# Optimization experiments

Measured on AMD Instinct MI355X. Metric: run time of the kernel, lower is better.

The kernel has to match this reference:

```python
import jax, jax.numpy as jnp
import numpy as np

H, B, N, D, VD, FFH = 8, 16, 512, 512, 64, 2048
NPICK = N // 2
NORM = 1.0 / np.sqrt(VD)


def _ha_encoder(h, W_query, W_key, W_val, W1, W2, W3, W4, W5, W6):
    # h: [B, N, D]; weights: [H, D, VD]
    np_ = NPICK
    pick, dlv = h[:, :np_], h[:, np_:]
    proj = lambda x, W: jnp.einsum('bnd,hdk->hbnk', x, W)
    Q, K, V = proj(h, W_query), proj(h, W_key), proj(h, W_val)
    Kp, Kd = K[:, :, :np_], K[:, :, np_:]   # shared projections (same W_key)
    Vp, Vd = V[:, :, :np_], V[:, :, np_:]
    Qp = proj(pick, W1); Qpap = proj(pick, W2); Qpad = proj(pick, W3)
    Qd = proj(dlv, W4);  Qdad = proj(dlv, W5);  Qdap = proj(dlv, W6)
    c_main = NORM * jnp.einsum('hbnk,hbmk->hbnm', Q, K)          # [H,B,N,N]
    c_pd = NORM * jnp.sum(Qp * Kd, -1)                           # [H,B,np] paired pick->delivery
    c_pap = NORM * jnp.einsum('hbnk,hbmk->hbnm', Qpap, Kp)       # pick -> all pick
    c_pad = NORM * jnp.einsum('hbnk,hbmk->hbnm', Qpad, Kd)       # pick -> all delivery
    c_dp = NORM * jnp.sum(Qd * Kp, -1)                           # paired delivery->pick
    c_dad = NORM * jnp.einsum('hbnk,hbmk->hbnm', Qdad, Kd)       # delivery -> all delivery
    c_dap = NORM * jnp.einsum('hbnk,hbmk->hbnm', Qdap, Kp)       # delivery -> all pick
    ninf1 = jnp.full((H, h.shape[0], np_), -jnp.inf, c_main.dtype)
    ninf2 = jnp.full((H, h.shape[0], np_, np_), -jnp.inf, c_main.dtype)
    col_pd = jnp.concatenate([c_pd, ninf1], 2)[..., None]        # [H,B,N,1]
    blk_pap = jnp.concatenate([c_pap, ninf2], 2)                 # [H,B,N,np]
    blk_pad = jnp.concatenate([c_pad, ninf2], 2)
    col_dp = jnp.concatenate([ninf1, c_dp], 2)[..., None]
    blk_dad = jnp.concatenate([ninf2, c_dad], 2)
    blk_dap = jnp.concatenate([ninf2, c_dap], 2)
    compat = jnp.concatenate([c_main, col_pd, blk_pap, blk_pad, col_dp, blk_dad, blk_dap], -1)
    a = jax.nn.softmax(compat, -1)                               # [H,B,N,N+2+4*np]
    zpad = jnp.zeros_like(Vd)
    V_add_d = jnp.concatenate([Vd, zpad], 2)                     # [H,B,N,VD]
    V_add_p = jnp.concatenate([zpad, Vp], 2)
    av = lambda w, v: jnp.einsum('hbnm,hbmv->hbnv', w, v)
    i = N
    heads = av(a[..., :N], V)
    heads = heads + a[..., i:i + 1] * V_add_d; i += 1
    heads = heads + av(a[..., i:i + np_], Vp); i += np_
    heads = heads + av(a[..., i:i + np_], Vd); i += np_
    heads = heads + a[..., i:i + 1] * V_add_p; i += 1
    heads = heads + av(a[..., i:i + np_], Vd); i += np_
    heads = heads + av(a[..., i:i + np_], Vp)
    return heads.transpose(1, 2, 0, 3).reshape(h.shape[0], N, H * VD)


def _split_heads(x):
    b, n, hd = x.shape
    return x.reshape(b, n, H, hd // H).transpose(0, 2, 1, 3)


def _mha(q, k, v):
    dk = q.shape[-1]
    w = jax.nn.softmax(jnp.einsum('bhnd,bhmd->bhnm', q, k) / np.sqrt(dk), -1)
    o = jnp.einsum('bhnm,bhmd->bhnd', w, v)
    b, hh, n, d = o.shape
    return o.transpose(0, 2, 1, 3).reshape(b, n, hh * d)


def _ff(x, w1, b1, w2, b2, a):
    return x + (jax.nn.relu(x @ w1 + b1) @ w2 + b2) * a


def _forward(x, W_query, W_key, W_val, W1_query, W2_query, W3_query, W4_query, W5_query, W6_query,
             Wq_w, Wk_w, Wv_w, Wq2p_w, Wq2d_w, Wk2_w, Wv2_w,
             comb_w, comb_b, comb2_w, comb2_b, comb3_w, comb3_b,
             alpha1, alpha2, alpha3,
             ff1_w1, ff1_b1, ff1_w2, ff1_b2, ffa1,
             ff2_w1, ff2_b1, ff2_w2, ff2_b2, ffa2,
             ff3_w1, ff3_b1, ff3_w2, ff3_b2, ffa3):
    # stage 1: heterogeneous attention block (combine_3 / AN3 / FF3)
    ha = _ha_encoder(x, W_query, W_key, W_val, W1_query, W2_query, W3_query, W4_query, W5_query, W6_query)
    out = x + (ha @ comb3_w + comb3_b) * alpha3
    out = _ff(out, ff3_w1, ff3_b1, ff3_w2, ff3_b2, ffa3)
    # stage 2: standard multi-head self-attention (combine / AN1 / FF1)
    q = _split_heads(out @ Wq_w); k = _split_heads(out @ Wk_w); v = _split_heads(out @ Wv_w)
    out = out + (_mha(q, k, v) @ comb_w + comb_b) * alpha1
    out = _ff(out, ff1_w1, ff1_b1, ff1_w2, ff1_b2, ffa1)
    # stage 3: pickup/delivery specific queries (combine_2 / AN2 / FF2)
    q2 = jnp.concatenate([out[:, :NPICK] @ Wq2p_w, out[:, NPICK:] @ Wq2d_w], 1)
    q2 = _split_heads(q2); k2 = _split_heads(out @ Wk2_w); v2 = _split_heads(out @ Wv2_w)
    out = out + (_mha(q2, k2, v2) @ comb2_w + comb2_b) * alpha2
    out = _ff(out, ff2_w1, ff2_b1, ff2_w2, ff2_b2, ffa2)
    return out


def setup_inputs() -> dict:
    key = jax.random.key(0)
    ks = jax.random.split(key, 64)
    it = iter(range(64))
    def nrm(shape):
        return jax.random.normal(ks[next(it)], shape, jnp.float32)
    def uni(shape):
        s = 1.0 / np.sqrt(shape[-1])  # torch init_parameters: uniform(-1/sqrt(size(-1)), ...)
        return jax.random.uniform(ks[next(it)], shape, jnp.float32, -s, s)
    d = {'x': nrm((B, N, D))}
    for n in ['W_query', 'W_key', 'W_val', 'W1_query', 'W2_query', 'W3_query', 'W4_query', 'W5_query', 'W6_query']:
        d[n] = uni((H, D, VD))
    for n in ['Wq_w', 'Wk_w', 'Wv_w', 'Wq2p_w', 'Wq2d_w', 'Wk2_w', 'Wv2_w']:
        d[n] = uni((D, H * VD))
    for n in ['comb_w', 'comb2_w', 'comb3_w']:
        d[n] = uni((H * VD, D))
    for n in ['comb_b', 'comb2_b', 'comb3_b']:
        d[n] = uni((D,))
    for n in ['alpha1', 'alpha2', 'alpha3']:
        d[n] = uni((1,))
    for i in ['1', '2', '3']:
        d['ff' + i + '_w1'] = uni((D, FFH))
        d['ff' + i + '_b1'] = uni((FFH,))
        d['ff' + i + '_w2'] = uni((FFH, D))
        d['ff' + i + '_b2'] = uni((D,))
        d['ffa' + i] = uni((1,))
    return d


def reference(x, W_query, W_key, W_val, W1_query, W2_query, W3_query, W4_query, W5_query, W6_query,
              Wq_w, Wk_w, Wv_w, Wq2p_w, Wq2d_w, Wk2_w, Wv2_w,
              comb_w, comb_b, comb2_w, comb2_b, comb3_w, comb3_b,
              alpha1, alpha2, alpha3,
              ff1_w1, ff1_b1, ff1_w2, ff1_b2, ffa1,
              ff2_w1, ff2_b1, ff2_w2, ff2_b2, ffa2,
              ff3_w1, ff3_b1, ff3_w2, ff3_b2, ffa3):
    return _forward(x, W_query, W_key, W_val, W1_query, W2_query, W3_query, W4_query, W5_query, W6_query,
                    Wq_w, Wk_w, Wv_w, Wq2p_w, Wq2d_w, Wk2_w, Wv2_w,
                    comb_w, comb_b, comb2_w, comb2_b, comb3_w, comb3_b,
                    alpha1, alpha2, alpha3,
                    ff1_w1, ff1_b1, ff1_w2, ff1_b2, ffa1,
                    ff2_w1, ff2_b1, ff2_w2, ff2_b2, ffa2,
                    ff3_w1, ff3_b1, ff3_w2, ff3_b2, ffa3)
```

## Files before the change

### kernel.cpp

```cpp
#include <hip/hip_runtime.h>
#include <math.h>

#define Hh 8
#define Bb 16
#define Nn 512
#define Dd 512
#define VDd 64
#define NPICKk 256
#define NORMF 0.125f
#define SCL2 0.1803368801f

typedef unsigned short ushortT;
typedef __bf16 bf16x8 __attribute__((ext_vector_type(8)));
typedef float f32x4 __attribute__((ext_vector_type(4)));

struct PtrsB { const ushortT* p[12]; };
struct PtrsD { ushortT* p[6]; };
struct Ptrs9 { const float* p[9]; };
struct Ptrs10 { const float* p[10]; };
struct Ptrs6 { const float* p[6]; };

__device__ inline ushortT f2bf(float f) {
    __bf16 h = (__bf16)f;
    union { __bf16 h; ushortT u; } v; v.h = h;
    return v.u;
}
__device__ inline float bf2f(ushortT u) {
    union { unsigned int u; float f; } v; v.u = ((unsigned int)u) << 16;
    return v.f;
}
__device__ inline float exp2fast(float x) {
#if __has_builtin(__builtin_amdgcn_exp2f)
    return __builtin_amdgcn_exp2f(x);
#else
    return exp2f(x);
#endif
}
__device__ inline void gload16(const void* gptr, void* ldsptr) {
    auto g = reinterpret_cast<const __attribute__((address_space(1))) unsigned int*>(
        reinterpret_cast<uintptr_t>(gptr));
    auto l = reinterpret_cast<__attribute__((address_space(3))) unsigned int*>(
        reinterpret_cast<uintptr_t>(ldsptr));
    __builtin_amdgcn_global_load_lds(g, l, 16, 0, 0);
}

#define LIX(r, g) (((r) << 6) + ((((g) ^ ((r) & 7))) << 3))

__global__ __launch_bounds__(256) void castx(const float* __restrict__ in,
                                             ushortT* __restrict__ out) {
    int i = blockIdx.x * 256 + threadIdx.x;
    float4 v = *(const float4*)&in[(size_t)i * 4];
    ushort4 o; o.x = f2bf(v.x); o.y = f2bf(v.y); o.z = f2bf(v.z); o.w = f2bf(v.w);
    *(ushort4*)&out[(size_t)i * 4] = o;
}

__device__ inline void tbody(const float* __restrict__ in, ushortT* __restrict__ out,
                             int in_ld, int out_ld, int r0, int c0) {
    __shared__ float T[64][65];
    int tr = threadIdx.x >> 4, tc4 = (threadIdx.x & 15) * 4;
#pragma unroll
    for (int p = 0; p < 4; ++p) {
        float4 v = *(const float4*)&in[(size_t)(r0 + tr + p * 16) * in_ld + c0 + tc4];
        T[tr + p * 16][tc4 + 0] = v.x; T[tr + p * 16][tc4 + 1] = v.y;
        T[tr + p * 16][tc4 + 2] = v.z; T[tr + p * 16][tc4 + 3] = v.w;
    }
    __syncthreads();
#pragma unroll
    for (int p = 0; p < 4; ++p) {
        int orow = c0 + tr + p * 16;
        int ocol = r0 + tc4;
        ushort4 o;
        o.x = f2bf(T[tc4 + 0][tr + p * 16]);
        o.y = f2bf(T[tc4 + 1][tr + p * 16]);
        o.z = f2bf(T[tc4 + 2][tr + p * 16]);
        o.w = f2bf(T[tc4 + 3][tr + p * 16]);
        *(ushort4*)&out[(size_t)orow * out_ld + ocol] = o;
    }
}

__global__ __launch_bounds__(256) void thead(Ptrs9 s, ushortT* __restrict__ dst) {
    int w = blockIdx.z >> 3, h = blockIdx.z & 7;
    tbody(s.p[w] + (size_t)h * 512 * 64,
          dst + (size_t)w * 262144 + (size_t)h * 64 * 512,
          64, 512, blockIdx.y * 64, 0);
}
__global__ __launch_bounds__(256) void tsq(Ptrs10 s, ushortT* __restrict__ dst) {
    tbody(s.p[blockIdx.z], dst + (size_t)blockIdx.z * 262144,
          512, 512, blockIdx.y * 64, blockIdx.x * 64);
}
__global__ __launch_bounds__(256) void tff(Ptrs6 s, ushortT* __restrict__ dst) {
    int z = blockIdx.z;
    if (z < 3) { if (blockIdx.y >= 8 || blockIdx.x >= 32) return; }
    else       { if (blockIdx.y >= 32 || blockIdx.x >= 8) return; }
    int in_ld = (z < 3) ? 2048 : 512;
    int out_ld = (z < 3) ? 512 : 2048;
    tbody(s.p[z], dst + (size_t)z * 1048576, in_ld, out_ld,
          blockIdx.y * 64, blockIdx.x * 64);
}

__global__ __launch_bounds__(256) void gemm_bf(
    PtrsB Bp, PtrsD Db, const ushortT* __restrict__ A, float* __restrict__ outF,
    int M, int N, int K, const float* __restrict__ bias,
    const float* __restrict__ res, const float* __restrict__ alpha,
    int do_relu, int nroute, int vtmask, int scmask)
{
    __shared__ __align__(16) ushortT As[2][128 * 64];
    __shared__ __align__(16) ushortT Bs[2][128 * 64];
    const int tid = threadIdx.x;
    const int wid = tid >> 6, lane = tid & 63;
    const int wm = wid >> 1, wn = wid & 1;
    const int l15 = lane & 15, l4 = lane >> 4;

    int bid = blockIdx.y * gridDim.x + blockIdx.x;
    int nwg = gridDim.x * gridDim.y;
    int q = nwg >> 3;
    int swz = (bid & 7) * q + (bid >> 3);
    int bx = swz % gridDim.x, by = swz / gridDim.x;

    const int r0 = by * 128, c0 = bx * 128;
    const int half = ((r0 & (Nn - 1)) >= NPICKk) ? 1 : 0;
    const ushortT* Bt = Bp.p[((c0 >> 9) << 1) | half];
    const int cB = nroute ? (c0 & 511) : c0;

    const ushortT* aSrc[4];
    const ushortT* bSrc[4];
    int offv[4];
#pragma unroll
    for (int i = 0; i < 4; ++i) {
        int off = wid * 4096 + i * 1024 + lane * 16;
        int row = off >> 7;
        int sg = ((off >> 4) & 7) ^ (row & 7);
        aSrc[i] = A + (size_t)(r0 + row) * K + sg * 8;
        bSrc[i] = Bt + (size_t)(cB + row) * K + sg * 8;
        offv[i] = off;
    }

    const int nkt = K >> 6;
#pragma unroll
    for (int i = 0; i < 4; ++i) {
        gload16(aSrc[i], (char*)As[0] + offv[i]);
        gload16(bSrc[i], (char*)Bs[0] + offv[i]);
    }
#pragma unroll
    for (int i = 0; i < 4; ++i) {
        gload16(aSrc[i] + 64, (char*)As[1] + offv[i]);
        gload16(bSrc[i] + 64, (char*)Bs[1] + offv[i]);
    }

    f32x4 acc[4][4] = {};

    for (int t = 0; t < nkt; ++t) {
        const int cur = t & 1;
        if (t == nkt - 1) asm volatile("s_waitcnt vmcnt(0)" ::: "memory");
        else              asm volatile("s_waitcnt vmcnt(8)" ::: "memory");
        __builtin_amdgcn_s_barrier();
        __builtin_amdgcn_sched_barrier(0);
        const ushortT* Ac = As[cur];
        const ushortT* Bc = Bs[cur];
        __builtin_amdgcn_s_setprio(1);
#pragma unroll
        for (int kk = 0; kk < 2; ++kk) {
            int g0 = kk * 4 + l4;
            bf16x8 af[4], bfv[4];
#pragma unroll
            for (int mi = 0; mi < 4; ++mi)
                af[mi] = *(const bf16x8*)&Ac[LIX(wm * 64 + mi * 16 + l15, g0)];
#pragma unroll
            for (int ni = 0; ni < 4; ++ni)
                bfv[ni] = *(const bf16x8*)&Bc[LIX(wn * 64 + ni * 16 + l15, g0)];
#pragma unroll
            for (int mi = 0; mi < 4; ++mi)
#pragma unroll
                for (int ni = 0; ni < 4; ++ni)
                    acc[mi][ni] = __builtin_amdgcn_mfma_f32_16x16x32_bf16(
                        bfv[ni], af[mi], acc[mi][ni], 0, 0, 0);
        }
        __builtin_amdgcn_s_setprio(0);
        __builtin_amdgcn_s_barrier();
        asm volatile("" ::: "memory");
        if (t + 2 < nkt) {
            int kt2 = (t + 2) << 6;
#pragma unroll
            for (int i = 0; i < 4; ++i) {
                gload16(aSrc[i] + kt2, (char*)As[cur] + offv[i]);
                gload16(bSrc[i] + kt2, (char*)Bs[cur] + offv[i]);
            }
        }
    }

    if (nroute) {
#pragma unroll
        for (int mi = 0; mi < 4; ++mi) {
            int row = r0 + wm * 64 + mi * 16 + l15;
#pragma unroll
            for (int ni = 0; ni < 4; ++ni) {
                int col = c0 + wn * 64 + ni * 16 + l4 * 4;
                int range = col >> 9, cc = col & 511;
                ushortT* d = Db.p[range];
                f32x4 a = acc[mi][ni];
                if ((scmask >> range) & 1) {
                    a[0] *= SCL2; a[1] *= SCL2; a[2] *= SCL2; a[3] *= SCL2;
                }
                if ((vtmask >> range) & 1) {
                    size_t vb = ((size_t)(row >> 9) * Hh + (cc >> 6)) * 64 + (cc & 63);
                    int tok = row & 511;
#pragma unroll
                    for (int r = 0; r < 4; ++r)
                        d[((vb + r) << 9) + tok] = f2bf(a[r]);
                } else {
                    ushort4 o;
                    o.x = f2bf(a[0]); o.y = f2bf(a[1]);
                    o.z = f2bf(a[2]); o.w = f2bf(a[3]);
                    *(ushort4*)&d[((size_t)row << 9) + cc] = o;
                }
            }
        }
    } else {
        const float alp = alpha ? alpha[0] : 1.0f;
        ushortT* outB = Db.p[0];
#pragma unroll
        for (int mi = 0; mi < 4; ++mi) {
            int row = r0 + wm * 64 + mi * 16 + l15;
#pragma unroll
            for (int ni = 0; ni < 4; ++ni) {
                int colb = c0 + wn * 64 + ni * 16 + l4 * 4;
                f32x4 a = acc[mi][ni];
                if (bias) {
                    float4 b4 = *(const float4*)&bias[colb];
                    a[0] += b4.x; a[1] += b4.y; a[2] += b4.z; a[3] += b4.w;
                }
                if (do_relu) {
#pragma unroll
                    for (int r = 0; r < 4; ++r) a[r] = fmaxf(a[r], 0.f);
                }
#pragma unroll
                for (int r = 0; r < 4; ++r) a[r] *= alp;
                size_t idx = (size_t)row * N + colb;
                if (res) {
                    float4 r4 = *(const float4*)&res[idx];
                    a[0] += r4.x; a[1] += r4.y; a[2] += r4.z; a[3] += r4.w;
                }
                if (outF)
                    *(float4*)&outF[idx] = make_float4(a[0], a[1], a[2], a[3]);
                if (outB) {
                    ushort4 o;
                    o.x = f2bf(a[0]); o.y = f2bf(a[1]);
                    o.z = f2bf(a[2]); o.w = f2bf(a[3]);
                    *(ushort4*)&outB[idx] = o;
                }
            }
        }
    }
}

__global__ __launch_bounds__(256) void gemm64(
    const ushortT* __restrict__ Bw, const ushortT* __restrict__ A,
    float* __restrict__ outF, ushortT* __restrict__ outB,
    int M, int N, int K, const float* __restrict__ bias,
    const float* __restrict__ resf, const ushortT* __restrict__ resb,
    const float* __restrict__ alpha, int do_relu)
{
    __shared__ __align__(16) ushortT As[2][64 * 64];
    __shared__ __align__(16) ushortT Bs[2][128 * 64];
    const int tid = threadIdx.x;
    const int wid = tid >> 6, lane = tid & 63;
    const int wm = wid >> 1, wn = wid & 1;
    const int l15 = lane & 15, l4 = lane >> 4;

    int bid = blockIdx.y * gridDim.x + blockIdx.x;
    int nwg = gridDim.x * gridDim.y;
    int q = nwg >> 3;
    int swz = (bid & 7) * q + (bid >> 3);
    int bx = swz % gridDim.x, by = swz / gridDim.x;
    const int r0 = by * 64, c0 = bx * 128;

    const ushortT* aSrc[2];
    int offA[2];
#pragma unroll
    for (int i = 0; i < 2; ++i) {
        int off = wid * 2048 + i * 1024 + lane * 16;
        int row = off >> 7;
        int sg = ((off >> 4) & 7) ^ (row & 7);
        aSrc[i] = A + (size_t)(r0 + row) * K + sg * 8;
        offA[i] = off;
    }
    const ushortT* bSrc[4];
    int offB[4];
#pragma unroll
    for (int i = 0; i < 4; ++i) {
        int off = wid * 4096 + i * 1024 + lane * 16;
        int row = off >> 7;
        int sg = ((off >> 4) & 7) ^ (row & 7);
        bSrc[i] = Bw + (size_t)(c0 + row) * K + sg * 8;
        offB[i] = off;
    }

    const int nkt = K >> 6;
#pragma unroll
    for (int i = 0; i < 2; ++i) gload16(aSrc[i], (char*)As[0] + offA[i]);
#pragma unroll
    for (int i = 0; i < 4; ++i) gload16(bSrc[i], (char*)Bs[0] + offB[i]);
#pragma unroll
    for (int i = 0; i < 2; ++i) gload16(aSrc[i] + 64, (char*)As[1] + offA[i]);
#pragma unroll
    for (int i = 0; i < 4; ++i) gload16(bSrc[i] + 64, (char*)Bs[1] + offB[i]);

    f32x4 acc[2][4] = {};

    for (int t = 0; t < nkt; ++t) {
        const int cur = t & 1;
        if (t == nkt - 1) asm volatile("s_waitcnt vmcnt(0)" ::: "memory");
        else              asm volatile("s_waitcnt vmcnt(6)" ::: "memory");
        __builtin_amdgcn_s_barrier();
        __builtin_amdgcn_sched_barrier(0);
        const ushortT* Ac = As[cur];
        const ushortT* Bc = Bs[cur];
        __builtin_amdgcn_s_setprio(1);
#pragma unroll
        for (int kk = 0; kk < 2; ++kk) {
            int g0 = kk * 4 + l4;
            bf16x8 af[2], bfv[4];
#pragma unroll
            for (int mi = 0; mi < 2; ++mi)
                af[mi] = *(const bf16x8*)&Ac[LIX(wm * 32 + mi * 16 + l15, g0)];
#pragma unroll
            for (int ni = 0; ni < 4; ++ni)
                bfv[ni] = *(const bf16x8*)&Bc[LIX(wn * 64 + ni * 16 + l15, g0)];
#pragma unroll
            for (int mi = 0; mi < 2; ++mi)
#pragma unroll
                for (int ni = 0; ni < 4; ++ni)
                    acc[mi][ni] = __builtin_amdgcn_mfma_f32_16x16x32_bf16(
                        bfv[ni], af[mi], acc[mi][ni], 0, 0, 0);
        }
        __builtin_amdgcn_s_setprio(0);
        __builtin_amdgcn_s_barrier();
        asm volatile("" ::: "memory");
        if (t + 2 < nkt) {
            int kt2 = (t + 2) << 6;
#pragma unroll
            for (int i = 0; i < 2; ++i) gload16(aSrc[i] + kt2, (char*)As[cur] + offA[i]);
#pragma unroll
            for (int i = 0; i < 4; ++i) gload16(bSrc[i] + kt2, (char*)Bs[cur] + offB[i]);
        }
    }

    const float alp = alpha ? alpha[0] : 1.0f;
#pragma unroll
    for (int mi = 0; mi < 2; ++mi) {
        int row = r0 + wm * 32 + mi * 16 + l15;
#pragma unroll
        for (int ni = 0; ni < 4; ++ni) {
            int colb = c0 + wn * 64 + ni * 16 + l4 * 4;
            f32x4 a = acc[mi][ni];
            if (bias) {
                float4 b4 = *(const float4*)&bias[colb];
                a[0] += b4.x; a[1] += b4.y; a[2] += b4.z; a[3] += b4.w;
            }
            if (do_relu) {
#pragma unroll
                for (int r = 0; r < 4; ++r) a[r] = fmaxf(a[r], 0.f);
            }
#pragma unroll
            for (int r = 0; r < 4; ++r) a[r] *= alp;
            size_t idx = (size_t)row * N + colb;
            if (resf) {
                float4 r4 = *(const float4*)&resf[idx];
                a[0] += r4.x; a[1] += r4.y; a[2] += r4.z; a[3] += r4.w;
            }
            if (resb) {
                ushort4 r4 = *(const ushort4*)&resb[idx];
                a[0] += bf2f(r4.x); a[1] += bf2f(r4.y);
                a[2] += bf2f(r4.z); a[3] += bf2f(r4.w);
            }
            if (outF)
                *(float4*)&outF[idx] = make_float4(a[0], a[1], a[2], a[3]);
            if (outB) {
                ushort4 o;
                o.x = f2bf(a[0]); o.y = f2bf(a[1]);
                o.z = f2bf(a[2]); o.w = f2bf(a[3]);
                *(ushort4*)&outB[idx] = o;
            }
        }
    }
}

__global__ __launch_bounds__(256) void diag_dot_bb(const ushortT* __restrict__ QD,
                                                   const ushortT* __restrict__ K,
                                                   float* __restrict__ Sdg) {
    int i = blockIdx.x * 256 + threadIdx.x;
    int h = i & 7, n = (i >> 3) & 511, b = i >> 12;
    int dix = (n < NPICKk) ? n + NPICKk : n - NPICKk;
    const ushortT* q = QD + (((size_t)(b * Nn + n) * Hh + h) << 6);
    const ushortT* k = K + (((size_t)(b * Nn + dix) * Hh + h) << 6);
    float s = 0.f;
#pragma unroll
    for (int d = 0; d < 64; d += 4) {
        ushort4 a = *(const ushort4*)(q + d);
        ushort4 c = *(const ushort4*)(k + d);
        s += bf2f(a.x) * bf2f(c.x) + bf2f(a.y) * bf2f(c.y)
           + bf2f(a.z) * bf2f(c.z) + bf2f(a.w) * bf2f(c.w);
    }
    Sdg[i] = s;
}

template <int HA>
__global__ __launch_bounds__(256) void attn10(
    const ushortT* __restrict__ Qm, const ushortT* __restrict__ Km,
    const ushortT* __restrict__ Vtm, const ushortT* __restrict__ QAm,
    const ushortT* __restrict__ QBm, const float* __restrict__ Sdg,
    ushortT* __restrict__ Out)
{
    __shared__ __align__(16) ushortT Ks[64 * 64];
    __shared__ __align__(16) ushortT Vs[64 * 64];
    __shared__ __align__(16) ushortT Pw[4][16 * 64];
    __shared__ float sdl[64];

    const int tid = threadIdx.x, wid = tid >> 6, lane = tid & 63;
    const int l15 = lane & 15, l4 = lane >> 4;

    const int p = blockIdx.x + (blockIdx.y << 3) + (blockIdx.z << 6);
    const int n0 = (((p >> 3) & 7)) << 6;
    const int g8 = (p & 7) | ((p >> 6) << 3);
    const int h = g8 & 7, b = g8 >> 3;
    const int bh = b * Hh + h;

    const size_t qrow = (((size_t)(b * Nn + n0 + wid * 16 + l15) * Hh + h) << 6);
    bf16x8 qf[2], xaf[2], xbf[2];
#pragma unroll
    for (int kk = 0; kk < 2; ++kk) {
        int g0 = kk * 4 + l4;
        qf[kk] = *(const bf16x8*)&Qm[qrow + g0 * 8];
        if (HA) {
            xaf[kk] = *(const bf16x8*)&QAm[qrow + g0 * 8];
            xbf[kk] = *(const bf16x8*)&QBm[qrow + g0 * 8];
        }
    }
    if (HA && tid < 64) sdl[tid] = Sdg[((size_t)(b * Nn + n0 + tid)) * Hh + h];
    const int td = (n0 < NPICKk) ? ((n0 + NPICKk) >> 6) : ((n0 - NPICKk) >> 6);

    const ushortT* kSrc[2]; ushortT* kDst[2];
    const ushortT* vSrc[2]; ushortT* vDst[2];
#pragma unroll
    for (int i = 0; i < 2; ++i) {
        int off = wid * 2048 + i * 1024 + lane * 16;
        int row = off >> 7, sg = ((off >> 4) & 7) ^ (row & 7);
        kSrc[i] = Km + (((size_t)(b * Nn + row) * Hh + h) << 6) + sg * 8;
        kDst[i] = (ushortT*)((char*)Ks + off);
        vSrc[i] = Vtm + (((size_t)(bh * 64 + row)) << 9) + sg * 8;
        vDst[i] = (ushortT*)((char*)Vs + off);
    }

    float M[4], Lp[4];
    f32x4 Oa[4] = {};
#pragma unroll
    for (int r = 0; r < 4; ++r) { M[r] = -INFINITY; Lp[r] = 0.f; }

    bf16x8 krbuf[2][2], vrbuf[2][2];
#pragma unroll
    for (int i = 0; i < 2; ++i) {
        krbuf[0][i] = *(const bf16x8*)kSrc[i];
        vrbuf[0][i] = *(const bf16x8*)vSrc[i];
    }

#pragma unroll
    for (int t = 0; t < 8; ++t) {
        const int cur = t & 1, nxt = cur ^ 1;
        __builtin_amdgcn_s_barrier();
#pragma unroll
        for (int i = 0; i < 2; ++i) {
            *(bf16x8*)kDst[i] = krbuf[cur][i];
            *(bf16x8*)vDst[i] = vrbuf[cur][i];
        }
        if (t < 7) {
#pragma unroll
            for (int i = 0; i < 2; ++i) {
                krbuf[nxt][i] = *(const bf16x8*)(kSrc[i] + (size_t)(t + 1) * (64 * Hh * VDd));
                vrbuf[nxt][i] = *(const bf16x8*)(vSrc[i] + (t + 1) * 64);
            }
        }
        asm volatile("s_waitcnt lgkmcnt(0)" ::: "memory");
        __builtin_amdgcn_s_barrier();
        __builtin_amdgcn_sched_barrier(0);

        __builtin_amdgcn_s_setprio(1);
        f32x4 s1[4] = {}, sX[4] = {};
#pragma unroll
        for (int kk = 0; kk < 2; ++kk) {
            bf16x8 aq = qf[kk];
            bf16x8 ax;
            if (HA) ax = (t >= 4) ? xbf[kk] : xaf[kk];
#pragma unroll
            for (int ni = 0; ni < 4; ++ni) {
                bf16x8 bk = *(const bf16x8*)&Ks[LIX(ni * 16 + l15, kk * 4 + l4)];
                s1[ni] = __builtin_amdgcn_mfma_f32_16x16x32_bf16(aq, bk, s1[ni], 0, 0, 0);
                if (HA)
                    sX[ni] = __builtin_amdgcn_mfma_f32_16x16x32_bf16(ax, bk, sX[ni], 0, 0, 0);
            }
        }
        __builtin_amdgcn_s_setprio(0);

        const bool dt = HA && (t == td);

        float mloc[4];
        bool grow = false;
#pragma unroll
        for (int r = 0; r < 4; ++r) {
            int rw = wid * 16 + l4 * 4 + r;
            float m = s1[0][r];
#pragma unroll
            for (int ni = 1; ni < 4; ++ni) m = fmaxf(m, s1[ni][r]);
            if (HA) {
#pragma unroll
                for (int ni = 0; ni < 4; ++ni) m = fmaxf(m, sX[ni][r]);
            }
            if (dt && l15 == l4 * 4 + r) m = fmaxf(m, sdl[rw]);
            mloc[r] = m;
            grow = grow || (m > M[r] + 8.f);
        }
        if (__any(grow)) {
#pragma unroll
            for (int r = 0; r < 4; ++r) {
                float m = mloc[r];
#pragma unroll
                for (int o = 8; o >= 1; o >>= 1) m = fmaxf(m, __shfl_xor(m, o, 16));
                float mn = fmaxf(M[r], m);
                float sc = exp2fast(M[r] - mn);
                M[r] = mn; Lp[r] *= sc;
#pragma unroll
                for (int ni = 0; ni < 4; ++ni) Oa[ni][r] *= sc;
            }
        }

#pragma unroll
        for (int r = 0; r < 4; ++r) {
            int rw = wid * 16 + l4 * 4 + r;
            float rs = 0.f;
#pragma unroll
            for (int ni = 0; ni < 4; ++ni) {
                float pv = exp2fast(s1[ni][r] - M[r]);
                if (HA) pv += exp2fast(sX[ni][r] - M[r]);
                if (dt && ni == wid && l15 == l4 * 4 + r) pv += exp2fast(sdl[rw] - M[r]);
                s1[ni][r] = pv;
                rs += pv;
            }
            Lp[r] += rs;
        }

#pragma unroll
        for (int ni = 0; ni < 4; ++ni)
#pragma unroll
            for (int r = 0; r < 4; ++r) {
                int prow = l4 * 4 + r;
                int col = ni * 16 + l15;
                Pw[wid][(prow << 6) + ((((col >> 3) ^ (prow & 7))) << 3) + (col & 7)] =
                    f2bf(s1[ni][r]);
            }

        __builtin_amdgcn_s_setprio(1);
#pragma unroll
        for (int kk = 0; kk < 2; ++kk) {
            int g0 = kk * 4 + l4;
            bf16x8 ap = *(const bf16x8*)&Pw[wid][LIX(l15, g0)];
#pragma unroll
            for (int ni = 0; ni < 4; ++ni) {
                bf16x8 bv = *(const bf16x8*)&Vs[LIX(ni * 16 + l15, g0)];
                Oa[ni] = __builtin_amdgcn_mfma_f32_16x16x32_bf16(ap, bv, Oa[ni], 0, 0, 0);
            }
        }
        __builtin_amdgcn_s_setprio(0);
    }

#pragma unroll
    for (int r = 0; r < 4; ++r) {
        float l = Lp[r];
#pragma unroll
        for (int o = 8; o >= 1; o >>= 1) l += __shfl_xor(l, o, 16);
        float inv = 1.0f / l;
        size_t obase = (((size_t)(b * Nn + n0 + wid * 16 + l4 * 4 + r) * Hh + h) << 6);
#pragma unroll
        for (int ni = 0; ni < 4; ++ni)
            Out[obase + ni * 16 + l15] = f2bf(Oa[ni][r] * inv);
    }
}

extern "C" void kernel_launch(void* const* d_in, const int* in_sizes, int n_in,
                              void* d_out, int out_size, void* d_ws, size_t ws_size,
                              hipStream_t stream)
{
    const float* x = (const float*)d_in[0];

    int dictOrder = (in_sizes[18] != 512);
    const float* comb_w  = (const float*)d_in[17];
    const float* comb2_w = (const float*)d_in[dictOrder ? 18 : 19];
    const float* comb3_w = (const float*)d_in[dictOrder ? 19 : 21];
    const float* comb_b  = (const float*)d_in[dictOrder ? 20 : 18];
    const float* comb2_b = (const float*)d_in[dictOrder ? 21 : 20];
    const float* comb3_b = (const float*)d_in[22];
    const float* alpha1 = (const float*)d_in[23];
    const float* alpha2 = (const float*)d_in[24];
    const float* alpha3 = (const float*)d_in[25];
    const float* ff1_w1 = (const float*)d_in[26];
    const float* ff1_b1 = (const float*)d_in[27];
    const float* ff1_w2 = (const float*)d_in[28];
    const float* ff1_b2 = (const float*)d_in[29];
    const float* ffa1   = (const float*)d_in[30];
    const float* ff2_w1 = (const float*)d_in[31];
    const float* ff2_b1 = (const float*)d_in[32];
    const float* ff2_w2 = (const float*)d_in[33];
    const float* ff2_b2 = (const float*)d_in[34];
    const float* ffa2   = (const float*)d_in[35];
    const float* ff3_w1 = (const float*)d_in[36];
    const float* ff3_b1 = (const float*)d_in[37];
    const float* ff3_w2 = (const float*)d_in[38];
    const float* ff3_b2 = (const float*)d_in[39];
    const float* ffa3   = (const float*)d_in[40];

    char* W = (char*)d_ws;
    ushortT* wbHead = (ushortT*)(W + 0);
    ushortT* wbMha  = (ushortT*)(W + 4718592);
    ushortT* wbComb = (ushortT*)(W + 8388608);
    ushortT* wbFf1  = (ushortT*)(W + 9961472);
    ushortT* wbFf2  = (ushortT*)(W + 16252928);
    ushortT* xbf    = (ushortT*)(W + 22544384);
    float*   Sd     = (float*)  (W + 30932992);
    ushortT* bufQ   = (ushortT*)(W + 31195136);
    ushortT* bufK   = (ushortT*)(W + 39583744);
    ushortT* bufVt  = (ushortT*)(W + 47972352);
    ushortT* bufQA  = (ushortT*)(W + 56360960);
    ushortT* bufQB  = (ushortT*)(W + 64749568);
    ushortT* bufQD  = (ushortT*)(W + 73138176);
    ushortT* hidden = (ushortT*)(W + 81526784);
    ushortT* curb   = (ushortT*)(W + 115081216);
    ushortT* bufHA  = xbf;
    float*   cur    = (float*)d_out;

    dim3 tb(256);
    const int TOK = Bb * Nn;
    const size_t WS = 512 * 512;
    const size_t WF = 2048 * 512;

    hipLaunchKernelGGL(castx, dim3(TOK * 512 / 1024), tb, 0, stream, x, xbf);
    {
        Ptrs9 s; for (int i = 0; i < 9; ++i) s.p[i] = (const float*)d_in[1 + i];
        hipLaunchKernelGGL(thead, dim3(1, 8, 72), tb, 0, stream, s, wbHead);
    }
    {
        Ptrs10 s;
        for (int i = 0; i < 7; ++i) s.p[i] = (const float*)d_in[10 + i];
        s.p[7] = comb_w; s.p[8] = comb2_w; s.p[9] = comb3_w;
        hipLaunchKernelGGL(tsq, dim3(8, 8, 10), tb, 0, stream, s, wbMha);
    }
    {
        Ptrs6 s;
        s.p[0] = ff1_w1; s.p[1] = ff2_w1; s.p[2] = ff3_w1;
        s.p[3] = ff1_w2; s.p[4] = ff2_w2; s.p[5] = ff3_w2;
        hipLaunchKernelGGL(tff, dim3(32, 32, 6), tb, 0, stream, s, wbFf1);
    }

    auto gemm = [&](PtrsB Bp, PtrsD Db, const ushortT* A, float* oF,
                    int M, int Ncc, int Kc, const float* bias, const float* res,
                    const float* alp, int relu, int nroute, int vtmask, int scmask) {
        hipLaunchKernelGGL(gemm_bf, dim3(Ncc / 128, M / 128), tb, 0, stream,
                           Bp, Db, A, oF, M, Ncc, Kc, bias, res, alp, relu, nroute,
                           vtmask, scmask);
    };
    auto g64 = [&](const ushortT* Bw, const ushortT* A, float* oF, ushortT* oB,
                   int M, int Ncc, int Kc, const float* bias, const float* resf,
                   const ushortT* resb, const float* alp, int relu) {
        hipLaunchKernelGGL(gemm64, dim3(Ncc / 128, M / 64), tb, 0, stream,
                           Bw, A, oF, oB, M, Ncc, Kc, bias, resf, resb, alp, relu);
    };
    auto uni = [&](const ushortT* w) { PtrsB b; for (int i = 0; i < 12; ++i) b.p[i] = w; return b; };
    auto d1 = [&](ushortT* d) { PtrsD dd = {}; dd.p[0] = d; return dd; };

    {
        PtrsB b;
        b.p[0] = b.p[1] = wbHead + 0 * WS;
        b.p[2] = b.p[3] = wbHead + 1 * WS;
        b.p[4] = b.p[5] = wbHead + 2 * WS;
        b.p[6] = wbHead + 4 * WS; b.p[7] = wbHead + 8 * WS;
        b.p[8] = wbHead + 5 * WS; b.p[9] = wbHead + 7 * WS;
        b.p[10] = wbHead + 3 * WS; b.p[11] = wbHead + 6 * WS;
        PtrsD d; d.p[0] = bufQ; d.p[1] = bufK; d.p[2] = bufVt;
        d.p[3] = bufQA; d.p[4] = bufQB; d.p[5] = bufQD;
        gemm(b, d, xbf, nullptr, TOK, 3072, 512, nullptr, nullptr, nullptr, 0, 6, 4, 57);
    }

    hipLaunchKernelGGL(diag_dot_bb, dim3(Bb * Nn * Hh / 256), tb, 0, stream, bufQD, bufK, Sd);
    hipLaunchKernelGGL((attn10<1>), dim3(Nn / 64, Hh, Bb), tb, 0, stream,
                       bufQ, bufK, bufVt, bufQA, bufQB, Sd, bufHA);

    g64(wbComb + 2 * WS, bufHA, nullptr, curb, TOK, 512, 512, comb3_b, x, nullptr, alpha3, 0);
    gemm(uni(wbFf1 + 2 * WF), d1(hidden), curb, nullptr, TOK, 2048, 512, ff3_b1, nullptr, nullptr, 1, 0, 0, 0);
    g64(wbFf2 + 2 * WF, hidden, nullptr, curb, TOK, 512, 2048, ff3_b2, nullptr, curb, ffa3, 0);

    {
        PtrsB b;
        b.p[0] = b.p[1] = wbMha + 0 * WS;
        b.p[2] = b.p[3] = wbMha + 1 * WS;
        b.p[4] = b.p[5] = wbMha + 2 * WS;
        PtrsD d = {}; d.p[0] = bufQ; d.p[1] = bufK; d.p[2] = bufVt;
        gemm(b, d, curb, nullptr, TOK, 1536, 512, nullptr, nullptr, nullptr, 0, 3, 4, 1);
    }
    hipLaunchKernelGGL((attn10<0>), dim3(Nn / 64, Hh, Bb), tb, 0, stream,
                       bufQ, bufK, bufVt, nullptr, nullptr, nullptr, bufHA);
    g64(wbComb + 0 * WS, bufHA, nullptr, curb, TOK, 512, 512, comb_b, nullptr, curb, alpha1, 0);
    gemm(uni(wbFf1 + 0 * WF), d1(hidden), curb, nullptr, TOK, 2048, 512, ff1_b1, nullptr, nullptr, 1, 0, 0, 0);
    g64(wbFf2 + 0 * WF, hidden, nullptr, curb, TOK, 512, 2048, ff1_b2, nullptr, curb, ffa1, 0);

    {
        PtrsB b;
        b.p[0] = wbMha + 3 * WS; b.p[1] = wbMha + 4 * WS;
        b.p[2] = b.p[3] = wbMha + 5 * WS;
        b.p[4] = b.p[5] = wbMha + 6 * WS;
        PtrsD d = {}; d.p[0] = bufQ; d.p[1] = bufK; d.p[2] = bufVt;
        gemm(b, d, curb, nullptr, TOK, 1536, 512, nullptr, nullptr, nullptr, 0, 3, 4, 1);
    }
    hipLaunchKernelGGL((attn10<0>), dim3(Nn / 64, Hh, Bb), tb, 0, stream,
                       bufQ, bufK, bufVt, nullptr, nullptr, nullptr, bufHA);
    g64(wbComb + 1 * WS, bufHA, nullptr, curb, TOK, 512, 512, comb2_b, nullptr, curb, alpha2, 0);
    gemm(uni(wbFf1 + 1 * WF), d1(hidden), curb, nullptr, TOK, 2048, 512, ff2_b1, nullptr, nullptr, 1, 0, 0, 0);
    g64(wbFf2 + 1 * WF, hidden, cur, nullptr, TOK, 512, 2048, ff2_b2, nullptr, curb, ffa2, 0);
}
```

Before: 426.4 us.

## Double attention query tile to 128 rows with 512-thread blocks sharing K/V

Each attention block now covers 128 query rows with 8 waves instead of 64 rows with 4, so every K/V tile staged in shared memory serves twice as many queries and each thread issues half as many global loads per tile. The grid shrinks to 512 blocks, and the diagonal-term indexing is adjusted per wave group. The cost is fewer blocks to spread across CUs and more waves waiting at each barrier.

```diff
diff --git a/kernel.cpp b/kernel.cpp
--- a/kernel.cpp
+++ b/kernel.cpp
@@ -405,7 +405,7 @@
 }
 
 template <int HA>
-__global__ __launch_bounds__(256) void attn10(
+__global__ __launch_bounds__(512) void attn11(
     const ushortT* __restrict__ Qm, const ushortT* __restrict__ Km,
     const ushortT* __restrict__ Vtm, const ushortT* __restrict__ QAm,
     const ushortT* __restrict__ QBm, const float* __restrict__ Sdg,
@@ -413,15 +413,15 @@
 {
     __shared__ __align__(16) ushortT Ks[64 * 64];
     __shared__ __align__(16) ushortT Vs[64 * 64];
-    __shared__ __align__(16) ushortT Pw[4][16 * 64];
-    __shared__ float sdl[64];
+    __shared__ __align__(16) ushortT Pw[8][16 * 64];
+    __shared__ float sdl[128];
 
     const int tid = threadIdx.x, wid = tid >> 6, lane = tid & 63;
     const int l15 = lane & 15, l4 = lane >> 4;
 
-    const int p = blockIdx.x + (blockIdx.y << 3) + (blockIdx.z << 6);
-    const int n0 = (((p >> 3) & 7)) << 6;
-    const int g8 = (p & 7) | ((p >> 6) << 3);
+    const int p = blockIdx.x + (blockIdx.y << 2) + (blockIdx.z << 5);
+    const int n0 = ((p >> 3) & 3) << 7;
+    const int g8 = (p & 7) | ((p >> 5) << 3);
     const int h = g8 & 7, b = g8 >> 3;
     const int bh = b * Hh + h;
 
@@ -436,48 +436,35 @@
             xbf[kk] = *(const bf16x8*)&QBm[qrow + g0 * 8];
         }
     }
-    if (HA && tid < 64) sdl[tid] = Sdg[((size_t)(b * Nn + n0 + tid)) * Hh + h];
-    const int td = (n0 < NPICKk) ? ((n0 + NPICKk) >> 6) : ((n0 - NPICKk) >> 6);
-
-    const ushortT* kSrc[2]; ushortT* kDst[2];
-    const ushortT* vSrc[2]; ushortT* vDst[2];
-#pragma unroll
-    for (int i = 0; i < 2; ++i) {
-        int off = wid * 2048 + i * 1024 + lane * 16;
-        int row = off >> 7, sg = ((off >> 4) & 7) ^ (row & 7);
-        kSrc[i] = Km + (((size_t)(b * Nn + row) * Hh + h) << 6) + sg * 8;
-        kDst[i] = (ushortT*)((char*)Ks + off);
-        vSrc[i] = Vtm + (((size_t)(bh * 64 + row)) << 9) + sg * 8;
-        vDst[i] = (ushortT*)((char*)Vs + off);
-    }
+    if (HA && tid < 128) sdl[tid] = Sdg[((size_t)(b * Nn + n0 + tid)) * Hh + h];
+    const int n0g = n0 + ((wid >> 2) << 6);
+    const int td = (n0g < NPICKk) ? ((n0g + NPICKk) >> 6) : ((n0g - NPICKk) >> 6);
+
+    const int off = wid * 1024 + lane * 16;
+    const int srow = off >> 7, sg = ((off >> 4) & 7) ^ (srow & 7);
+    const ushortT* kSrc = Km + (((size_t)(b * Nn + srow) * Hh + h) << 6) + sg * 8;
+    ushortT* kDst = (ushortT*)((char*)Ks + off);
+    const ushortT* vSrc = Vtm + (((size_t)(bh * 64 + srow)) << 9) + sg * 8;
+    ushortT* vDst = (ushortT*)((char*)Vs + off);
 
     float M[4], Lp[4];
     f32x4 Oa[4] = {};
 #pragma unroll
     for (int r = 0; r < 4; ++r) { M[r] = -INFINITY; Lp[r] = 0.f; }
 
-    bf16x8 krbuf[2][2], vrbuf[2][2];
-#pragma unroll
-    for (int i = 0; i < 2; ++i) {
-        krbuf[0][i] = *(const bf16x8*)kSrc[i];
-        vrbuf[0][i] = *(const bf16x8*)vSrc[i];
-    }
+    bf16x8 krbuf[2], vrbuf[2];
+    krbuf[0] = *(const bf16x8*)kSrc;
+    vrbuf[0] = *(const bf16x8*)vSrc;
 
 #pragma unroll
     for (int t = 0; t < 8; ++t) {
         const int cur = t & 1, nxt = cur ^ 1;
         __builtin_amdgcn_s_barrier();
-#pragma unroll
-        for (int i = 0; i < 2; ++i) {
-            *(bf16x8*)kDst[i] = krbuf[cur][i];
-            *(bf16x8*)vDst[i] = vrbuf[cur][i];
-        }
+        *(bf16x8*)kDst = krbuf[cur];
+        *(bf16x8*)vDst = vrbuf[cur];
         if (t < 7) {
-#pragma unroll
-            for (int i = 0; i < 2; ++i) {
-                krbuf[nxt][i] = *(const bf16x8*)(kSrc[i] + (size_t)(t + 1) * (64 * Hh * VDd));
-                vrbuf[nxt][i] = *(const bf16x8*)(vSrc[i] + (t + 1) * 64);
-            }
+            krbuf[nxt] = *(const bf16x8*)(kSrc + (size_t)(t + 1) * (64 * Hh * VDd));
+            vrbuf[nxt] = *(const bf16x8*)(vSrc + (t + 1) * 64);
         }
         asm volatile("s_waitcnt lgkmcnt(0)" ::: "memory");
         __builtin_amdgcn_s_barrier();
@@ -540,7 +527,8 @@
             for (int ni = 0; ni < 4; ++ni) {
                 float pv = exp2fast(s1[ni][r] - M[r]);
                 if (HA) pv += exp2fast(sX[ni][r] - M[r]);
-                if (dt && ni == wid && l15 == l4 * 4 + r) pv += exp2fast(sdl[rw] - M[r]);
+                if (dt && ni == (wid & 3) && l15 == l4 * 4 + r)
+                    pv += exp2fast(sdl[rw] - M[r]);
                 s1[ni][r] = pv;
                 rs += pv;
             }
@@ -688,7 +676,7 @@
     }
 
     hipLaunchKernelGGL(diag_dot_bb, dim3(Bb * Nn * Hh / 256), tb, 0, stream, bufQD, bufK, Sd);
-    hipLaunchKernelGGL((attn10<1>), dim3(Nn / 64, Hh, Bb), tb, 0, stream,
+    hipLaunchKernelGGL((attn11<1>), dim3(Nn / 128, Hh, Bb), dim3(512), 0, stream,
                        bufQ, bufK, bufVt, bufQA, bufQB, Sd, bufHA);
 
     g64(wbComb + 2 * WS, bufHA, nullptr, curb, TOK, 512, 512, comb3_b, x, nullptr, alpha3, 0);
@@ -703,7 +691,7 @@
         PtrsD d = {}; d.p[0] = bufQ; d.p[1] = bufK; d.p[2] = bufVt;
         gemm(b, d, curb, nullptr, TOK, 1536, 512, nullptr, nullptr, nullptr, 0, 3, 4, 1);
     }
-    hipLaunchKernelGGL((attn10<0>), dim3(Nn / 64, Hh, Bb), tb, 0, stream,
+    hipLaunchKernelGGL((attn11<0>), dim3(Nn / 128, Hh, Bb), dim3(512), 0, stream,
                        bufQ, bufK, bufVt, nullptr, nullptr, nullptr, bufHA);
     g64(wbComb + 0 * WS, bufHA, nullptr, curb, TOK, 512, 512, comb_b, nullptr, curb, alpha1, 0);
     gemm(uni(wbFf1 + 0 * WF), d1(hidden), curb, nullptr, TOK, 2048, 512, ff1_b1, nullptr, nullptr, 1, 0, 0, 0);
@@ -717,7 +705,7 @@
         PtrsD d = {}; d.p[0] = bufQ; d.p[1] = bufK; d.p[2] = bufVt;
         gemm(b, d, curb, nullptr, TOK, 1536, 512, nullptr, nullptr, nullptr, 0, 3, 4, 1);
     }
-    hipLaunchKernelGGL((attn10<0>), dim3(Nn / 64, Hh, Bb), tb, 0, stream,
+    hipLaunchKernelGGL((attn11<0>), dim3(Nn / 128, Hh, Bb), dim3(512), 0, stream,
                        bufQ, bufK, bufVt, nullptr, nullptr, nullptr, bufHA);
     g64(wbComb + 1 * WS, bufHA, nullptr, curb, TOK, 512, 512, comb2_b, nullptr, curb, alpha2, 0);
     gemm(uni(wbFf1 + 1 * WF), d1(hidden), curb, nullptr, TOK, 2048, 512, ff2_b1, nullptr, nullptr, 1, 0, 0, 0);
```

New measurement: 415.1 us (median of 2 runs). 2.7% less time.
